# Performance work log

Hardware: AMD Instinct MI355X
Metric: run time of the kernel (lower is better)

The kernel has to match this reference:

```python
import jax, jax.numpy as jnp
import numpy as np
from jax.ops import segment_sum

N = 100000      # nodes
E = 1600000     # edges
G = 128         # graphs in batch
D = 128         # input (embedding) dim
H = 128         # hidden dim
WALK = 16       # random-walk length
PED = 16        # PE embed dim
L = 5           # GNN layers
OUT = 10        # classes
EPS = 1e-5      # batchnorm eps


def setup_inputs() -> dict:
    key = jax.random.key(0)
    ks = jax.random.split(key, 32)
    f = lambda k, shp: (jax.random.normal(k, shp, dtype=jnp.float32) * 0.05)
    inp = {
        'x': jnp.zeros((N,), dtype=jnp.int64) if jax.config.jax_enable_x64 else jnp.zeros((N,), dtype=jnp.int32),
        'edge_index': jax.random.randint(ks[0], (2, E), 0, N),
        'batch': jnp.sort(jax.random.randint(ks[1], (N,), 0, G)),
        'emb_table': f(ks[2], (1, D)),
        'pe_w': f(ks[3], (WALK, PED)), 'pe_b': f(ks[4], (PED,)),
        'proj_w': f(ks[5], (D + PED, H)), 'proj_b': f(ks[6], (H,)),
        'gin_w1': f(ks[7], (L, H, H)), 'gin_b1': f(ks[8], (L, H)),
        'gin_w2': f(ks[9], (L, H, H)), 'gin_b2': f(ks[10], (L, H)),
        'bn_g': jnp.ones((L, H), jnp.float32), 'bn_b': jnp.zeros((L, H), jnp.float32),
        'ffn_w1': f(ks[11], (L, H, 2 * H)), 'ffn_b1': f(ks[12], (L, 2 * H)),
        'ffn_w2': f(ks[13], (L, 2 * H, H)), 'ffn_b2': f(ks[14], (L, H)),
        'ffn_bn_g': jnp.ones((L, H), jnp.float32), 'ffn_bn_b': jnp.zeros((L, H), jnp.float32),
        'out_w1': f(ks[15], (H, H)), 'out_b1': f(ks[16], (H,)),
        'out_w2': f(ks[17], (H, OUT)), 'out_b2': f(ks[18], (OUT,)),
    }
    return inp


def _batchnorm(h, g, b):
    # BatchNorm1d forward with batch statistics (training-mode math)
    mu = jnp.mean(h, axis=0)
    var = jnp.var(h, axis=0)
    return (h - mu) * jax.lax.rsqrt(var + EPS) * g + b


def _forward(emb_table, pe_w, pe_b, proj_w, proj_b, gin_w1, gin_b1, gin_w2, gin_b2,
             bn_g, bn_b, ffn_w1, ffn_b1, ffn_w2, ffn_b2, ffn_bn_g, ffn_bn_b,
             out_w1, out_b1, out_w2, out_b2, x, edge_index, batch):
    h0 = emb_table[x]                                # [N, D] (all indices are 0)

    # ---- RandomWalkPositionalEncoding (vectorized scatter-add per step) ----
    row0, col0 = edge_index[0], edge_index[1]
    loops = jnp.arange(N)
    row = jnp.concatenate([row0, loops])
    col = jnp.concatenate([col0, loops])             # self loops appended
    deg = segment_sum(jnp.ones(row.shape, jnp.float32), col, num_segments=N)
    dinv = jnp.where(deg > 0, jax.lax.rsqrt(jnp.maximum(deg, 1.0)), 0.0)
    norm_e = dinv[row] * dinv[col]                   # [E+N]

    cnt = segment_sum(jnp.ones((N,), jnp.float32), batch, num_segments=G)
    prob = 1.0 / jnp.maximum(cnt, 1.0)[batch]        # per-graph uniform init

    def rw_step(p, _):
        new_p = segment_sum(p[row] * norm_e, col, num_segments=N)
        return new_p * 0.9 + p * 0.1, p

    _, rw = jax.lax.scan(rw_step, prob, None, length=WALK)   # [WALK, N]
    pe = rw.T @ pe_w + pe_b                          # [N, PED]

    # ---- input projection ----
    h = jnp.concatenate([h0, pe], axis=-1) @ proj_w + proj_b # [N, H]

    # ---- stacked GIN layers with BN, residual and FFN (dropout = eval identity) ----
    for i in range(L):
        res = h
        agg = segment_sum(h[row0], col0, num_segments=N) + h  # GIN: (1+eps)x + sum_j x_j, eps=0
        z = jax.nn.relu(agg @ gin_w1[i] + gin_b1[i]) @ gin_w2[i] + gin_b2[i]
        z = jax.nn.relu(_batchnorm(z, bn_g[i], bn_b[i]))
        h = z + res
        res2 = h
        f = jax.nn.relu(h @ ffn_w1[i] + ffn_b1[i]) @ ffn_w2[i] + ffn_b2[i]
        h = _batchnorm(f + res2, ffn_bn_g[i], ffn_bn_b[i])

    # ---- global mean pooling + MLP head ----
    gsum = segment_sum(h, batch, num_segments=G)
    g = gsum / jnp.maximum(cnt, 1.0)[:, None]        # [G, H]
    out = jax.nn.relu(g @ out_w1 + out_b1) @ out_w2 + out_b2
    return out                                        # [G, OUT]


def reference(x, edge_index, batch, emb_table, pe_w, pe_b, proj_w, proj_b,
              gin_w1, gin_b1, gin_w2, gin_b2, bn_g, bn_b, ffn_w1, ffn_b1,
              ffn_w2, ffn_b2, ffn_bn_g, ffn_bn_b, out_w1, out_b1, out_w2, out_b2):
    return _forward(emb_table, pe_w, pe_b, proj_w, proj_b, gin_w1, gin_b1, gin_w2,
                    gin_b2, bn_g, bn_b, ffn_w1, ffn_b1, ffn_w2, ffn_b2,
                    ffn_bn_g, ffn_bn_b, out_w1, out_b1, out_w2, out_b2,
                    x, edge_index, batch)
```

## Files before the change

kernel.cpp:

```cpp
#include <hip/hip_runtime.h>
#include <math.h>

#define NN 100000
#define NE 1600000
#define NG 128
#define HD 128
#define WLK 16
#define NL 5
#define NOUT 10
#define BNEPS 1e-5f
#define CDIV(a,b) (((a)+(b)-1)/(b))

#define NBKT 782
#define NEB 400
#define EPB 4000
#define NSCAN (NBKT*NEB)
#define NSB CDIV(NSCAN,1024)
#define NBM 782

typedef float f32x4 __attribute__((ext_vector_type(4)));
typedef _Float16 f16x8 __attribute__((ext_vector_type(8)));
typedef unsigned short ushort_t;
typedef unsigned int uint_t;

__device__ __forceinline__ ushort_t f2h(float x) {
    union { _Float16 h; ushort_t u; } c;
    c.h = (_Float16)x;
    return c.u;
}
__device__ __forceinline__ float h2f(ushort_t u) {
    union { ushort_t u; _Float16 h; } c;
    c.u = u;
    return (float)c.h;
}

__global__ void k_cnt(const int* __restrict__ batch, int* __restrict__ cnt,
                      int* __restrict__ goff) {
    int g = threadIdx.x;
    if (g >= NG) return;
    int lo0 = 0, hi0 = NN;
    while (lo0 < hi0) { int m = (lo0 + hi0) >> 1; if (batch[m] < g) lo0 = m + 1; else hi0 = m; }
    int lo1 = lo0, hi1 = NN;
    while (lo1 < hi1) { int m = (lo1 + hi1) >> 1; if (batch[m] < g + 1) lo1 = m + 1; else hi1 = m; }
    cnt[g] = lo1 - lo0;
    goff[g] = lo0;
}

__global__ void k_bhist(const int* __restrict__ col0, int* __restrict__ bhist) {
    __shared__ int hist[NBKT];
    for (int i = threadIdx.x; i < NBKT; i += 256) hist[i] = 0;
    __syncthreads();
    int e0 = blockIdx.x * EPB;
    for (int e = e0 + threadIdx.x; e < e0 + EPB; e += 256) atomicAdd(&hist[col0[e] >> 7], 1);
    __syncthreads();
    for (int i = threadIdx.x; i < NBKT; i += 256) bhist[i * NEB + blockIdx.x] = hist[i];
}

__global__ void k_gscan1(const int* __restrict__ in, int* __restrict__ bsum) {
    __shared__ int sm[256];
    int base = blockIdx.x * 1024 + threadIdx.x * 4;
    int s = 0;
#pragma unroll
    for (int i = 0; i < 4; ++i) { int e = base + i; if (e < NSCAN) s += in[e]; }
    sm[threadIdx.x] = s; __syncthreads();
    for (int st = 128; st > 0; st >>= 1) {
        if (threadIdx.x < st) sm[threadIdx.x] += sm[threadIdx.x + st];
        __syncthreads();
    }
    if (threadIdx.x == 0) bsum[blockIdx.x] = sm[0];
}

__global__ void k_scan2(int* __restrict__ blksum, int nblk) {
    __shared__ int sm[512];
    int t = threadIdx.x;
    int x = (t < nblk) ? blksum[t] : 0;
    sm[t] = x; __syncthreads();
    for (int s = 1; s < 512; s <<= 1) {
        int v = (t >= s) ? sm[t - s] : 0;
        __syncthreads();
        sm[t] += v;
        __syncthreads();
    }
    if (t < nblk) blksum[t] = sm[t] - x;
}

__global__ void k_gscan3(const int* __restrict__ in, const int* __restrict__ bsum,
                         int* __restrict__ out) {
    __shared__ int sm[256];
    int t = threadIdx.x;
    int base = blockIdx.x * 1024 + t * 4;
    int v[4]; int s = 0;
#pragma unroll
    for (int i = 0; i < 4; ++i) { int e = base + i; v[i] = (e < NSCAN) ? in[e] : 0; s += v[i]; }
    sm[t] = s; __syncthreads();
    for (int st = 1; st < 256; st <<= 1) {
        int x = (t >= st) ? sm[t - st] : 0;
        __syncthreads();
        sm[t] += x;
        __syncthreads();
    }
    int excl = sm[t] - s + bsum[blockIdx.x];
#pragma unroll
    for (int i = 0; i < 4; ++i) { int e = base + i; if (e < NSCAN) { out[e] = excl; excl += v[i]; } }
}

__global__ void k_escatter(const int* __restrict__ row0, const int* __restrict__ col0,
                           const int* __restrict__ boffs, int2* __restrict__ epair) {
    __shared__ int cur[NBKT];
    for (int i = threadIdx.x; i < NBKT; i += 256) cur[i] = boffs[i * NEB + blockIdx.x];
    __syncthreads();
    int e0 = blockIdx.x * EPB;
    for (int e = e0 + threadIdx.x; e < e0 + EPB; e += 256) {
        int c = col0[e], r = row0[e];
        int pos = atomicAdd(&cur[c >> 7], 1);
        epair[pos] = make_int2(c, r);
    }
}

__global__ void k_bucket(const int2* __restrict__ epair, const int* __restrict__ boffs,
                         int* __restrict__ rowptr, int* __restrict__ deg,
                         int* __restrict__ esrc) {
    __shared__ int cnt_[128], scn[128], cur_[128];
    int bkt = blockIdx.x, t = threadIdx.x;
    int bs = boffs[bkt * NEB];
    int be = (bkt + 1 < NBKT) ? boffs[(bkt + 1) * NEB] : NE;
    if (t < 128) cnt_[t] = 0;
    __syncthreads();
    for (int e = bs + t; e < be; e += 256) atomicAdd(&cnt_[epair[e].x & 127], 1);
    __syncthreads();
    int c = (t < 128) ? cnt_[t] : 0;
    if (t < 128) scn[t] = c;
    __syncthreads();
    for (int st = 1; st < 128; st <<= 1) {
        int x = (t >= st && t < 128) ? scn[t - st] : 0;
        __syncthreads();
        if (t < 128) scn[t] += x;
        __syncthreads();
    }
    if (t < 128) {
        int excl = scn[t] - c;
        int node = bkt * 128 + t;
        if (node < NN) { rowptr[node] = bs + excl; deg[node] = c; }
        cur_[t] = bs + excl;
    }
    if (bkt == NBKT - 1 && t == 0) rowptr[NN] = NE;
    __syncthreads();
    for (int e = bs + t; e < be; e += 256) {
        int2 p = epair[e];
        int pos = atomicAdd(&cur_[p.x & 127], 1);
        esrc[pos] = p.y;
    }
}

__global__ void k_init_pe(const int* __restrict__ deg, const int* __restrict__ batch,
                          const int* __restrict__ cnt, float* __restrict__ dinv,
                          float* __restrict__ p, float* __restrict__ pd) {
    int v = blockIdx.x * 256 + threadIdx.x;
    if (v >= NN) return;
    float dv = rsqrtf((float)(deg[v] + 1));
    dinv[v] = dv;
    float pv = 1.0f / fmaxf((float)cnt[batch[v]], 1.0f);
    p[v] = pv; pd[v] = pv * dv;
}

__global__ void k_rw_step(const float* __restrict__ pin, const float* __restrict__ pdin,
                          const int* __restrict__ rowptr, const int* __restrict__ esrc,
                          const float* __restrict__ dinv, float* __restrict__ rwslice,
                          float* __restrict__ pout, float* __restrict__ pdout) {
    int v = blockIdx.x * 256 + threadIdx.x;
    if (v >= NN) return;
    int b = rowptr[v], e = rowptr[v + 1];
    float a0 = 0.f, a1 = 0.f, a2 = 0.f, a3 = 0.f;
    int i = b;
    for (; i + 4 <= e; i += 4) {
        int s0 = esrc[i], s1 = esrc[i + 1], s2 = esrc[i + 2], s3 = esrc[i + 3];
        a0 += pdin[s0]; a1 += pdin[s1]; a2 += pdin[s2]; a3 += pdin[s3];
    }
    for (; i < e; ++i) a0 += pdin[esrc[i]];
    float s = (a0 + a1) + (a2 + a3);
    float dv = dinv[v];
    float pv = pin[v];
    float np = s * dv + pv * dv * dv;
    float nxt = 0.9f * np + 0.1f * pv;
    rwslice[v] = pv;
    pout[v] = nxt;
    pdout[v] = nxt * dv;
}

__global__ void k_mc1(const float* __restrict__ emb, const float* __restrict__ pe_w,
                      const float* __restrict__ pe_b, const float* __restrict__ proj_w,
                      const float* __restrict__ proj_b, float* __restrict__ M,
                      float* __restrict__ c1, float* __restrict__ bnA0,
                      float* __restrict__ bnB0) {
    int j = threadIdx.x;
    bnA0[j] = 1.f; bnB0[j] = 0.f;
    float c0 = proj_b[j];
    for (int d = 0; d < HD; ++d) c0 += emb[d] * proj_w[d * HD + j];
    for (int w = 0; w < WLK; ++w) c0 += pe_b[w] * proj_w[(HD + w) * HD + j];
    c1[j] = c0;
    for (int s = 0; s < WLK; ++s) {
        float m = 0.f;
        for (int w = 0; w < WLK; ++w) m += pe_w[s * WLK + w] * proj_w[(HD + w) * HD + j];
        M[s * HD + j] = m;
    }
}

__global__ void k_proj(const float* __restrict__ rw, const float* __restrict__ M,
                       const float* __restrict__ c1, uint2* __restrict__ th4) {
    int idx = blockIdx.x * 256 + threadIdx.x;
    if (idx >= NN * 32) return;
    int v = idx >> 5, cg = (idx & 31) * 4;
    float4 acc = *(const float4*)&c1[cg];
#pragma unroll
    for (int s = 0; s < WLK; ++s) {
        float r = rw[s * NN + v];
        float4 m = *(const float4*)&M[s * HD + cg];
        acc.x += r * m.x; acc.y += r * m.y; acc.z += r * m.z; acc.w += r * m.w;
    }
    th4[idx] = make_uint2((uint_t)f2h(acc.x) | ((uint_t)f2h(acc.y) << 16),
                          (uint_t)f2h(acc.z) | ((uint_t)f2h(acc.w) << 16));
}

__global__ void k_prepw(const float* __restrict__ g1, const float* __restrict__ g2,
                        const float* __restrict__ f1, const float* __restrict__ f2,
                        ushort_t* __restrict__ wt1, ushort_t* __restrict__ wt2,
                        ushort_t* __restrict__ wt3, ushort_t* __restrict__ wt4) {
    int i = blockIdx.x * 256 + threadIdx.x;
    if (i < 81920) {
        int l = i >> 14, rem = i & 16383, n = rem >> 7, k = rem & 127;
        wt1[i] = f2h(g1[l * 16384 + k * 128 + n]);
    } else if (i < 163840) {
        int j = i - 81920;
        int l = j >> 14, rem = j & 16383, n = rem >> 7, k = rem & 127;
        wt2[j] = f2h(g2[l * 16384 + k * 128 + n]);
    } else if (i < 327680) {
        int j = i - 163840;
        int l = j >> 15, rem = j & 32767, n = rem >> 7, k = rem & 127;
        wt3[j] = f2h(f1[l * 32768 + k * 256 + n]);
    } else {
        int j = i - 327680;
        int l = j >> 15, rem = j & 32767, n = rem >> 8, k = rem & 255;
        wt4[j] = f2h(f2[l * 32768 + k * 128 + n]);
    }
}

__global__ void k_aggb(const uint_t* __restrict__ th2, const int* __restrict__ rowptr,
                       const int* __restrict__ esrc, const float* __restrict__ bnA0,
                       const float* __restrict__ bnB0, uint_t* __restrict__ aggb2) {
    int wave = threadIdx.x >> 6, lane = threadIdx.x & 63;
    int v = blockIdx.x * 4 + wave;
    if (v >= NN) return;
    uint_t u = th2[(size_t)v * 64 + lane];
    float sx[8], sy[8];
#pragma unroll
    for (int k = 0; k < 8; ++k) { sx[k] = 0.f; sy[k] = 0.f; }
    sx[0] = h2f((ushort_t)(u & 0xFFFFu)); sy[0] = h2f((ushort_t)(u >> 16));
    int b = rowptr[v], e = rowptr[v + 1];
    int i = b;
    for (; i + 8 <= e; i += 8) {
        int idx[8]; uint_t x[8];
#pragma unroll
        for (int k = 0; k < 8; ++k) idx[k] = esrc[i + k];
#pragma unroll
        for (int k = 0; k < 8; ++k) x[k] = th2[(size_t)idx[k] * 64 + lane];
#pragma unroll
        for (int k = 0; k < 8; ++k) {
            sx[k] += h2f((ushort_t)(x[k] & 0xFFFFu));
            sy[k] += h2f((ushort_t)(x[k] >> 16));
        }
    }
    for (; i < e; ++i) {
        uint_t x = th2[(size_t)esrc[i] * 64 + lane];
        sx[0] += h2f((ushort_t)(x & 0xFFFFu)); sy[0] += h2f((ushort_t)(x >> 16));
    }
    float fx = ((sx[0] + sx[1]) + (sx[2] + sx[3])) + ((sx[4] + sx[5]) + (sx[6] + sx[7]));
    float fy = ((sy[0] + sy[1]) + (sy[2] + sy[3])) + ((sy[4] + sy[5]) + (sy[6] + sy[7]));
    float2 A = *(const float2*)&bnA0[lane * 2];
    float2 B = *(const float2*)&bnB0[lane * 2];
    float cf = (float)(e - b + 1);
    float ox = A.x * fx + cf * B.x;
    float oy = A.y * fy + cf * B.y;
    aggb2[(size_t)v * 64 + lane] = (uint_t)f2h(ox) | ((uint_t)f2h(oy) << 16);
}

#define GLDK 136
__global__ __launch_bounds__(256)
void k_gin(const ushort_t* __restrict__ A, const ushort_t* __restrict__ W1T,
           const ushort_t* __restrict__ W2T, const float* __restrict__ b1,
           const float* __restrict__ b2, ushort_t* __restrict__ z2h,
           float* __restrict__ partS, float* __restrict__ partQ) {
    __shared__ ushort_t As[128 * GLDK];
    __shared__ ushort_t Ws[64 * GLDK];
    __shared__ float sS[128], sQ[128];
    const int tid = threadIdx.x;
    const int w = tid >> 6, l = tid & 63;
    const int lm = l & 15, lq = l >> 4;
    const int rw0 = w * 32;
    const int vr0 = blockIdx.x * 128;
    if (tid < 128) { sS[tid] = 0.f; sQ[tid] = 0.f; }

#pragma unroll
    for (int it = 0; it < 8; ++it) {
        int f = it * 256 + tid;
        int row = f >> 4, sl = f & 15;
        uint4 a = make_uint4(0, 0, 0, 0);
        int vr = vr0 + row;
        if (vr < NN) a = *(const uint4*)&A[(size_t)vr * HD + sl * 8];
        *(uint4*)&As[row * GLDK + sl * 8] = a;
    }

    f32x4 z1a[2][2][4] = {};
    for (int c = 0; c < 2; ++c) {
        __syncthreads();
#pragma unroll
        for (int it = 0; it < 4; ++it) {
            int f = it * 256 + tid;
            int row = f >> 4, sl = f & 15;
            *(uint4*)&Ws[row * GLDK + sl * 8] =
                *(const uint4*)&W1T[(size_t)(c * 64 + row) * HD + sl * 8];
        }
        __syncthreads();
#pragma unroll
        for (int kk = 0; kk < 128; kk += 32) {
            f16x8 af[2], bf[4];
#pragma unroll
            for (int i = 0; i < 2; ++i)
                af[i] = *(const f16x8*)&As[(rw0 + i * 16 + lm) * GLDK + kk + lq * 8];
#pragma unroll
            for (int j = 0; j < 4; ++j)
                bf[j] = *(const f16x8*)&Ws[(j * 16 + lm) * GLDK + kk + lq * 8];
#pragma unroll
            for (int i = 0; i < 2; ++i)
#pragma unroll
                for (int j = 0; j < 4; ++j)
                    z1a[c][i][j] = __builtin_amdgcn_mfma_f32_16x16x32_f16(af[i], bf[j], z1a[c][i][j], 0, 0, 0);
        }
    }
    __syncthreads();

#pragma unroll
    for (int c = 0; c < 2; ++c)
#pragma unroll
        for (int j = 0; j < 4; ++j) {
            int col = c * 64 + j * 16 + lm;
            float bj = b1[col];
#pragma unroll
            for (int i = 0; i < 2; ++i)
#pragma unroll
                for (int r = 0; r < 4; ++r) {
                    int row = rw0 + i * 16 + lq * 4 + r;
                    As[row * GLDK + col] = f2h(fmaxf(z1a[c][i][j][r] + bj, 0.f));
                }
        }

    f32x4 z2a[2][2][4] = {};
    for (int c2 = 0; c2 < 2; ++c2) {
        __syncthreads();
#pragma unroll
        for (int it = 0; it < 4; ++it) {
            int f = it * 256 + tid;
            int row = f >> 4, sl = f & 15;
            *(uint4*)&Ws[row * GLDK + sl * 8] =
                *(const uint4*)&W2T[(size_t)(c2 * 64 + row) * HD + sl * 8];
        }
        __syncthreads();
#pragma unroll
        for (int kk = 0; kk < 128; kk += 32) {
            f16x8 af[2], bf[4];
#pragma unroll
            for (int i = 0; i < 2; ++i)
                af[i] = *(const f16x8*)&As[(rw0 + i * 16 + lm) * GLDK + kk + lq * 8];
#pragma unroll
            for (int j = 0; j < 4; ++j)
                bf[j] = *(const f16x8*)&Ws[(j * 16 + lm) * GLDK + kk + lq * 8];
#pragma unroll
            for (int i = 0; i < 2; ++i)
#pragma unroll
                for (int j = 0; j < 4; ++j)
                    z2a[c2][i][j] = __builtin_amdgcn_mfma_f32_16x16x32_f16(af[i], bf[j], z2a[c2][i][j], 0, 0, 0);
        }
    }

    float ls[2][4] = {}, lsq[2][4] = {};
#pragma unroll
    for (int c2 = 0; c2 < 2; ++c2)
#pragma unroll
        for (int j = 0; j < 4; ++j) {
            int col = c2 * 64 + j * 16 + lm;
            float bj = b2[col];
#pragma unroll
            for (int i = 0; i < 2; ++i)
#pragma unroll
                for (int r = 0; r < 4; ++r) {
                    int vr = vr0 + rw0 + i * 16 + lq * 4 + r;
                    if (vr < NN) {
                        float x = z2a[c2][i][j][r] + bj;
                        ls[c2][j] += x; lsq[c2][j] += x * x;
                        z2h[(size_t)vr * HD + col] = f2h(x);
                    }
                }
        }
#pragma unroll
    for (int c2 = 0; c2 < 2; ++c2)
#pragma unroll
        for (int j = 0; j < 4; ++j) {
            atomicAdd(&sS[c2 * 64 + j * 16 + lm], ls[c2][j]);
            atomicAdd(&sQ[c2 * 64 + j * 16 + lm], lsq[c2][j]);
        }
    __syncthreads();
    if (tid < 128) {
        partS[(size_t)tid * NBM + blockIdx.x] = sS[tid];
        partQ[(size_t)tid * NBM + blockIdx.x] = sQ[tid];
    }
}

__global__ __launch_bounds__(256)
void k_ffn1(const ushort_t* __restrict__ th, const ushort_t* __restrict__ z2h,
            const ushort_t* __restrict__ W3T, const float* __restrict__ b3,
            const float* __restrict__ bnA0, const float* __restrict__ bnB0,
            const float* __restrict__ bnA1, const float* __restrict__ bnB1,
            float* __restrict__ hmid, ushort_t* __restrict__ f1h) {
    __shared__ ushort_t As[128 * GLDK];
    __shared__ ushort_t Ws[64 * GLDK];
    __shared__ float sA0[128], sB0[128], sA1[128], sB1[128];
    const int tid = threadIdx.x;
    const int w = tid >> 6, l = tid & 63;
    const int lm = l & 15, lq = l >> 4;
    const int rw0 = w * 32;
    const int vr0 = blockIdx.x * 128;

    if (tid < 128) {
        sA0[tid] = bnA0[tid]; sB0[tid] = bnB0[tid];
        sA1[tid] = bnA1[tid]; sB1[tid] = bnB1[tid];
    }
    __syncthreads();

#pragma unroll
    for (int it = 0; it < 8; ++it) {
        int f = it * 256 + tid;
        int row = f >> 4, sl = f & 15;
        int vr = vr0 + row;
        uint4 o = make_uint4(0, 0, 0, 0);
        if (vr < NN) {
            uint4 tv = *(const uint4*)&th[(size_t)vr * HD + sl * 8];
            uint4 zv = *(const uint4*)&z2h[(size_t)vr * HD + sl * 8];
            uint_t tu[4] = {tv.x, tv.y, tv.z, tv.w};
            uint_t zu[4] = {zv.x, zv.y, zv.z, zv.w};
            float hm[8];
            uint_t ou[4];
#pragma unroll
            for (int m = 0; m < 4; ++m) {
                int ch0 = sl * 8 + m * 2;
                float t0 = h2f((ushort_t)(tu[m] & 0xFFFFu));
                float t1 = h2f((ushort_t)(tu[m] >> 16));
                float z0 = h2f((ushort_t)(zu[m] & 0xFFFFu));
                float z1 = h2f((ushort_t)(zu[m] >> 16));
                float h0 = sA0[ch0] * t0 + sB0[ch0] + fmaxf(sA1[ch0] * z0 + sB1[ch0], 0.f);
                float h1 = sA0[ch0 + 1] * t1 + sB0[ch0 + 1] + fmaxf(sA1[ch0 + 1] * z1 + sB1[ch0 + 1], 0.f);
                hm[m * 2] = h0; hm[m * 2 + 1] = h1;
                ou[m] = (uint_t)f2h(h0) | ((uint_t)f2h(h1) << 16);
            }
            o = make_uint4(ou[0], ou[1], ou[2], ou[3]);
            *(float4*)&hmid[(size_t)vr * HD + sl * 8] = make_float4(hm[0], hm[1], hm[2], hm[3]);
            *(float4*)&hmid[(size_t)vr * HD + sl * 8 + 4] = make_float4(hm[4], hm[5], hm[6], hm[7]);
        }
        *(uint4*)&As[row * GLDK + sl * 8] = o;
    }

    for (int c = 0; c < 4; ++c) {
        __syncthreads();
#pragma unroll
        for (int it = 0; it < 4; ++it) {
            int f = it * 256 + tid;
            int row = f >> 4, sl = f & 15;
            *(uint4*)&Ws[row * GLDK + sl * 8] =
                *(const uint4*)&W3T[(size_t)(c * 64 + row) * HD + sl * 8];
        }
        __syncthreads();
        f32x4 acc[2][4] = {};
#pragma unroll
        for (int kk = 0; kk < 128; kk += 32) {
            f16x8 af[2], bf[4];
#pragma unroll
            for (int i = 0; i < 2; ++i)
                af[i] = *(const f16x8*)&As[(rw0 + i * 16 + lm) * GLDK + kk + lq * 8];
#pragma unroll
            for (int j = 0; j < 4; ++j)
                bf[j] = *(const f16x8*)&Ws[(j * 16 + lm) * GLDK + kk + lq * 8];
#pragma unroll
            for (int i = 0; i < 2; ++i)
#pragma unroll
                for (int j = 0; j < 4; ++j)
                    acc[i][j] = __builtin_amdgcn_mfma_f32_16x16x32_f16(af[i], bf[j], acc[i][j], 0, 0, 0);
        }
#pragma unroll
        for (int j = 0; j < 4; ++j) {
            int col = c * 64 + j * 16 + lm;
            float bj = b3[col];
#pragma unroll
            for (int i = 0; i < 2; ++i)
#pragma unroll
                for (int r = 0; r < 4; ++r) {
                    int vr = vr0 + rw0 + i * 16 + lq * 4 + r;
                    if (vr < NN)
                        f1h[(size_t)vr * 256 + col] = f2h(fmaxf(acc[i][j][r] + bj, 0.f));
                }
        }
    }
}

template <int K, bool RELU, bool OUTH16, bool ADDRES, bool DOSTATS>
__global__ __launch_bounds__(256, 2)
void k_mgemm(const ushort_t* __restrict__ A, const ushort_t* __restrict__ WT,
             const float* __restrict__ bias, ushort_t* __restrict__ Ch,
             float* __restrict__ Cf, const float* __restrict__ res,
             float* __restrict__ partS, float* __restrict__ partQ, int ncols) {
    constexpr int LDK = 72;
    __shared__ ushort_t As[128 * LDK];
    __shared__ ushort_t Ws[128 * LDK];
    __shared__ float sS[128], sQ[128];
    const int tid = threadIdx.x;
    const int w = tid >> 6, l = tid & 63;
    const int lm = l & 15, lq = l >> 4;
    const int rb = (w >> 1) * 64, cbw = (w & 1) * 64;
    const int vr0 = blockIdx.x * 128;
    const int cb = blockIdx.y * 128;
    f32x4 acc[4][4] = {};

    for (int kt = 0; kt < K / 64; ++kt) {
        __syncthreads();
#pragma unroll
        for (int it = 0; it < 4; ++it) {
            int f = it * 256 + tid;
            int row = f >> 3, sl = f & 7;
            uint4 a = make_uint4(0, 0, 0, 0);
            int vr = vr0 + row;
            if (vr < NN) a = *(const uint4*)&A[(size_t)vr * K + kt * 64 + sl * 8];
            *(uint4*)&As[row * LDK + sl * 8] = a;
            uint4 wv = *(const uint4*)&WT[(size_t)(cb + row) * K + kt * 64 + sl * 8];
            *(uint4*)&Ws[row * LDK + sl * 8] = wv;
        }
        __syncthreads();
#pragma unroll
        for (int kk = 0; kk < 64; kk += 32) {
            f16x8 af[4], bf[4];
#pragma unroll
            for (int i = 0; i < 4; ++i)
                af[i] = *(const f16x8*)&As[(rb + i * 16 + lm) * LDK + kk + lq * 8];
#pragma unroll
            for (int j = 0; j < 4; ++j)
                bf[j] = *(const f16x8*)&Ws[(cbw + j * 16 + lm) * LDK + kk + lq * 8];
#pragma unroll
            for (int i = 0; i < 4; ++i)
#pragma unroll
                for (int j = 0; j < 4; ++j)
                    acc[i][j] = __builtin_amdgcn_mfma_f32_16x16x32_f16(af[i], bf[j], acc[i][j], 0, 0, 0);
        }
    }

    float bcol[4];
#pragma unroll
    for (int j = 0; j < 4; ++j) bcol[j] = bias[cb + cbw + j * 16 + lm];
    if (DOSTATS && tid < 128) { sS[tid] = 0.f; sQ[tid] = 0.f; }
    __syncthreads();
    float ls[4] = {0, 0, 0, 0}, lsq[4] = {0, 0, 0, 0};
#pragma unroll
    for (int i = 0; i < 4; ++i) {
#pragma unroll
        for (int r = 0; r < 4; ++r) {
            int vr = vr0 + rb + i * 16 + lq * 4 + r;
            if (vr < NN) {
#pragma unroll
                for (int j = 0; j < 4; ++j) {
                    float x = acc[i][j][r] + bcol[j];
                    if (RELU) x = fmaxf(x, 0.f);
                    int c = cb + cbw + j * 16 + lm;
                    if (ADDRES) x += res[(size_t)vr * ncols + c];
                    if (DOSTATS) { ls[j] += x; lsq[j] += x * x; }
                    if (OUTH16) Ch[(size_t)vr * ncols + c] = f2h(x);
                    else        Cf[(size_t)vr * ncols + c] = x;
                }
            }
        }
    }
    if (DOSTATS) {
#pragma unroll
        for (int j = 0; j < 4; ++j) {
            atomicAdd(&sS[cbw + j * 16 + lm], ls[j]);
            atomicAdd(&sQ[cbw + j * 16 + lm], lsq[j]);
        }
        __syncthreads();
        if (tid < 128) {
            partS[(size_t)(cb + tid) * NBM + blockIdx.x] = sS[tid];
            partQ[(size_t)(cb + tid) * NBM + blockIdx.x] = sQ[tid];
        }
    }
}

__global__ void k_bnparm(const float* __restrict__ partS, const float* __restrict__ partQ,
                         const float* __restrict__ g, const float* __restrict__ b,
                         float* __restrict__ bnA, float* __restrict__ bnB) {
    __shared__ float smS[256], smQ[256];
    int c = blockIdx.x, t = threadIdx.x;
    float s = 0.f, q = 0.f;
    for (int i = t; i < NBM; i += 256) {
        s += partS[(size_t)c * NBM + i];
        q += partQ[(size_t)c * NBM + i];
    }
    smS[t] = s; smQ[t] = q; __syncthreads();
    for (int st = 128; st > 0; st >>= 1) {
        if (t < st) { smS[t] += smS[t + st]; smQ[t] += smQ[t + st]; }
        __syncthreads();
    }
    if (t == 0) {
        float mu = smS[0] * (1.0f / NN);
        float var = smQ[0] * (1.0f / NN) - mu * mu;
        float inv = rsqrtf(var + BNEPS);
        float a = g[c] * inv;
        bnA[c] = a;
        bnB[c] = b[c] - mu * a;
    }
}

__global__ void k_pool(const uint2* __restrict__ th4, const int* __restrict__ goff,
                       const int* __restrict__ cnt, float* __restrict__ gsum) {
    __shared__ float4 sm[256];
    int g = blockIdx.x >> 2, sub = blockIdx.x & 3;
    int n0 = goff[g], n = cnt[g];
    int cg = threadIdx.x & 31, rl = threadIdx.x >> 5;
    float4 acc = make_float4(0.f, 0.f, 0.f, 0.f);
    for (int r = sub * 8 + rl; r < n; r += 32) {
        uint2 v = th4[(size_t)(n0 + r) * 32 + cg];
        acc.x += h2f((ushort_t)(v.x & 0xFFFFu));
        acc.y += h2f((ushort_t)(v.x >> 16));
        acc.z += h2f((ushort_t)(v.y & 0xFFFFu));
        acc.w += h2f((ushort_t)(v.y >> 16));
    }
    sm[threadIdx.x] = acc; __syncthreads();
    for (int st = 128; st >= 32; st >>= 1) {
        if (threadIdx.x < st) {
            float4 o = sm[threadIdx.x + st];
            sm[threadIdx.x].x += o.x; sm[threadIdx.x].y += o.y;
            sm[threadIdx.x].z += o.z; sm[threadIdx.x].w += o.w;
        }
        __syncthreads();
    }
    if (threadIdx.x < 32) {
        float4 v = sm[threadIdx.x];
        atomicAdd(&gsum[g * HD + cg * 4 + 0], v.x);
        atomicAdd(&gsum[g * HD + cg * 4 + 1], v.y);
        atomicAdd(&gsum[g * HD + cg * 4 + 2], v.z);
        atomicAdd(&gsum[g * HD + cg * 4 + 3], v.w);
    }
}

__global__ void k_head(const float* __restrict__ gsum, const int* __restrict__ cnt,
                       const float* __restrict__ bnA0, const float* __restrict__ bnB0,
                       const float* __restrict__ w1, const float* __restrict__ b1,
                       const float* __restrict__ w2, const float* __restrict__ b2,
                       float* __restrict__ out) {
    __shared__ float gv[HD], av[HD];
    int gid = blockIdx.x, t = threadIdx.x;
    float c = fmaxf((float)cnt[gid], 1.0f);
    gv[t] = bnA0[t] * (gsum[gid * HD + t] / c) + bnB0[t];
    __syncthreads();
    float a = b1[t];
    for (int k = 0; k < HD; ++k) a += gv[k] * w1[k * HD + t];
    av[t] = fmaxf(a, 0.f);
    __syncthreads();
    if (t < NOUT) {
        float o = b2[t];
        for (int k = 0; k < HD; ++k) o += av[k] * w2[k * NOUT + t];
        out[gid * NOUT + t] = o;
    }
}

static constexpr size_t AL(size_t x) { return (x + 511) & ~(size_t)511; }
static constexpr size_t OFF_HMID   = 0;
static constexpr size_t OFF_TH     = OFF_HMID   + AL((size_t)NN * HD * 4);
static constexpr size_t OFF_SHARE  = OFF_TH     + AL((size_t)NN * HD * 2);
static constexpr size_t SZ_SHARE   = AL((size_t)NN * 256 * 2);
static constexpr size_t OFF_Z2     = OFF_SHARE  + SZ_SHARE;
static constexpr size_t OFF_RW     = OFF_Z2     + AL((size_t)NN * HD * 2);
static constexpr size_t OFF_P0     = OFF_RW     + AL((size_t)WLK * NN * 4);
static constexpr size_t OFF_P1     = OFF_P0     + AL((size_t)NN * 4);
static constexpr size_t OFF_PD0    = OFF_P1     + AL((size_t)NN * 4);
static constexpr size_t OFF_PD1    = OFF_PD0    + AL((size_t)NN * 4);
static constexpr size_t OFF_DINV   = OFF_PD1    + AL((size_t)NN * 4);
static constexpr size_t OFF_ESRC   = OFF_DINV   + AL((size_t)NN * 4);
static constexpr size_t OFF_ROWPTR = OFF_ESRC   + AL((size_t)NE * 4);
static constexpr size_t OFF_DEG    = OFF_ROWPTR + AL((size_t)(NN + 1) * 4);
static constexpr size_t OFF_BHIST  = OFF_DEG    + AL((size_t)NN * 4);
static constexpr size_t OFF_BOFFS  = OFF_BHIST  + AL((size_t)NSCAN * 4);
static constexpr size_t OFF_BSUM   = OFF_BOFFS  + AL((size_t)NSCAN * 4);
static constexpr size_t OFF_WT1    = OFF_BSUM   + AL(512 * 4);
static constexpr size_t OFF_WT2    = OFF_WT1    + AL((size_t)5 * 16384 * 2);
static constexpr size_t OFF_WT3    = OFF_WT2    + AL((size_t)5 * 16384 * 2);
static constexpr size_t OFF_WT4    = OFF_WT3    + AL((size_t)5 * 32768 * 2);
static constexpr size_t OFF_PARTS  = OFF_WT4    + AL((size_t)5 * 32768 * 2);
static constexpr size_t OFF_PARTQ  = OFF_PARTS  + AL((size_t)128 * NBM * 4);
static constexpr size_t OFF_BNA0   = OFF_PARTQ  + AL((size_t)128 * NBM * 4);
static constexpr size_t OFF_BNB0   = OFF_BNA0   + AL(128 * 4);
static constexpr size_t OFF_BNA1   = OFF_BNB0   + AL(128 * 4);
static constexpr size_t OFF_BNB1   = OFF_BNA1   + AL(128 * 4);
static constexpr size_t OFF_M      = OFF_BNB1   + AL(128 * 4);
static constexpr size_t OFF_C1     = OFF_M      + AL((size_t)WLK * HD * 4);
static constexpr size_t OFF_CNT    = OFF_C1     + AL(HD * 4);
static constexpr size_t OFF_GOFF   = OFF_CNT    + AL(NG * 4);
static constexpr size_t OFF_GSUM   = OFF_GOFF   + AL(NG * 4);
static constexpr size_t ZERO_BYTES = (size_t)NG * HD * 4;

extern "C" void kernel_launch(void* const* d_in, const int* in_sizes, int n_in,
                              void* d_out, int out_size, void* d_ws, size_t ws_size,
                              hipStream_t stream) {
    const int* eidx = (const int*)d_in[1];
    const int* row0 = eidx;
    const int* col0 = eidx + NE;
    const int* batch = (const int*)d_in[2];
    const float* emb = (const float*)d_in[3];
    const float* pe_w = (const float*)d_in[4];
    const float* pe_b = (const float*)d_in[5];
    const float* proj_w = (const float*)d_in[6];
    const float* proj_b = (const float*)d_in[7];
    const float* gin_w1 = (const float*)d_in[8];
    const float* gin_b1 = (const float*)d_in[9];
    const float* gin_w2 = (const float*)d_in[10];
    const float* gin_b2 = (const float*)d_in[11];
    const float* bn_g = (const float*)d_in[12];
    const float* bn_b = (const float*)d_in[13];
    const float* ffn_w1 = (const float*)d_in[14];
    const float* ffn_b1 = (const float*)d_in[15];
    const float* ffn_w2 = (const float*)d_in[16];
    const float* ffn_b2 = (const float*)d_in[17];
    const float* ffn_bn_g = (const float*)d_in[18];
    const float* ffn_bn_b = (const float*)d_in[19];
    const float* out_w1 = (const float*)d_in[20];
    const float* out_b1 = (const float*)d_in[21];
    const float* out_w2 = (const float*)d_in[22];
    const float* out_b2 = (const float*)d_in[23];
    float* out = (float*)d_out;

    char* ws = (char*)d_ws;
    float*    hmid  = (float*)(ws + OFF_HMID);
    ushort_t* th    = (ushort_t*)(ws + OFF_TH);
    ushort_t* aggh  = (ushort_t*)(ws + OFF_SHARE);
    ushort_t* f1h   = (ushort_t*)(ws + OFF_SHARE);
    ushort_t* z2h   = (ushort_t*)(ws + OFF_Z2);
    int2*     epair = (int2*)(ws + OFF_SHARE);
    float*    rw    = (float*)(ws + OFF_RW);
    float*    p0    = (float*)(ws + OFF_P0);
    float*    p1    = (float*)(ws + OFF_P1);
    float*    pd0   = (float*)(ws + OFF_PD0);
    float*    pd1   = (float*)(ws + OFF_PD1);
    float*    dinv  = (float*)(ws + OFF_DINV);
    int*      esrc  = (int*)(ws + OFF_ESRC);
    int*      rowptr= (int*)(ws + OFF_ROWPTR);
    int*      deg   = (int*)(ws + OFF_DEG);
    int*      bhist = (int*)(ws + OFF_BHIST);
    int*      boffs = (int*)(ws + OFF_BOFFS);
    int*      bsum  = (int*)(ws + OFF_BSUM);
    ushort_t* wt1   = (ushort_t*)(ws + OFF_WT1);
    ushort_t* wt2   = (ushort_t*)(ws + OFF_WT2);
    ushort_t* wt3   = (ushort_t*)(ws + OFF_WT3);
    ushort_t* wt4   = (ushort_t*)(ws + OFF_WT4);
    float*    partS = (float*)(ws + OFF_PARTS);
    float*    partQ = (float*)(ws + OFF_PARTQ);
    float*    bnA0  = (float*)(ws + OFF_BNA0);
    float*    bnB0  = (float*)(ws + OFF_BNB0);
    float*    bnA1  = (float*)(ws + OFF_BNA1);
    float*    bnB1  = (float*)(ws + OFF_BNB1);
    float*    M     = (float*)(ws + OFF_M);
    float*    c1    = (float*)(ws + OFF_C1);
    int*      cnt   = (int*)(ws + OFF_CNT);
    int*      goff  = (int*)(ws + OFF_GOFF);
    float*    gsum  = (float*)(ws + OFF_GSUM);

    const int NB = CDIV(NN, 256);
    const int NBV = CDIV(NN * 32, 256);

    hipMemsetAsync(ws + OFF_GSUM, 0, ZERO_BYTES, stream);

    k_cnt<<<1, 128, 0, stream>>>(batch, cnt, goff);
    k_bhist<<<NEB, 256, 0, stream>>>(col0, bhist);
    k_gscan1<<<NSB, 256, 0, stream>>>(bhist, bsum);
    k_scan2<<<1, 512, 0, stream>>>(bsum, NSB);
    k_gscan3<<<NSB, 256, 0, stream>>>(bhist, bsum, boffs);
    k_escatter<<<NEB, 256, 0, stream>>>(row0, col0, boffs, epair);
    k_bucket<<<NBKT, 256, 0, stream>>>(epair, boffs, rowptr, deg, esrc);

    k_init_pe<<<NB, 256, 0, stream>>>(deg, batch, cnt, dinv, p0, pd0);
    k_mc1<<<1, 128, 0, stream>>>(emb, pe_w, pe_b, proj_w, proj_b, M, c1, bnA0, bnB0);
    k_prepw<<<1920, 256, 0, stream>>>(gin_w1, gin_w2, ffn_w1, ffn_w2, wt1, wt2, wt3, wt4);
    for (int s = 0; s < WLK; ++s) {
        const float* pin = (s & 1) ? p1 : p0;
        const float* pdin = (s & 1) ? pd1 : pd0;
        float* pout = (s & 1) ? p0 : p1;
        float* pdout = (s & 1) ? pd0 : pd1;
        k_rw_step<<<NB, 256, 0, stream>>>(pin, pdin, rowptr, esrc, dinv,
                                          rw + (size_t)s * NN, pout, pdout);
    }
    k_proj<<<NBV, 256, 0, stream>>>(rw, M, c1, (uint2*)th);

    dim3 g1(NBM, 1);
    for (int i = 0; i < NL; ++i) {
        k_aggb<<<CDIV(NN, 4), 256, 0, stream>>>((const uint_t*)th, rowptr, esrc,
                                                bnA0, bnB0, (uint_t*)aggh);
        k_gin<<<NBM, 256, 0, stream>>>(aggh, wt1 + (size_t)i * 16384, wt2 + (size_t)i * 16384,
                                       gin_b1 + i * HD, gin_b2 + i * HD, z2h, partS, partQ);
        k_bnparm<<<128, 256, 0, stream>>>(partS, partQ, bn_g + i * HD, bn_b + i * HD, bnA1, bnB1);
        k_ffn1<<<NBM, 256, 0, stream>>>(th, z2h, wt3 + (size_t)i * 32768, ffn_b1 + i * 256,
                                        bnA0, bnB0, bnA1, bnB1, hmid, f1h);
        k_mgemm<256, false, true, true, true><<<g1, 256, 0, stream>>>(
            f1h, wt4 + (size_t)i * 32768, ffn_b2 + i * HD, th, nullptr, hmid,
            partS, partQ, 128);
        k_bnparm<<<128, 256, 0, stream>>>(partS, partQ, ffn_bn_g + i * HD, ffn_bn_b + i * HD,
                                          bnA0, bnB0);
    }

    k_pool<<<NG * 4, 256, 0, stream>>>((const uint2*)th, goff, cnt, gsum);
    k_head<<<NG, 128, 0, stream>>>(gsum, cnt, bnA0, bnB0, out_w1, out_b1, out_w2, out_b2, out);
}
```

Before: 1.585 ms.

## Fuse neighbor aggregation into GIN GEMM and recompute FFN residual instead of storing fp32

```diff
diff --git a/kernel.cpp b/kernel.cpp
--- a/kernel.cpp
+++ b/kernel.cpp
@@ -170,14 +170,19 @@
     int v = blockIdx.x * 256 + threadIdx.x;
     if (v >= NN) return;
     int b = rowptr[v], e = rowptr[v + 1];
-    float a0 = 0.f, a1 = 0.f, a2 = 0.f, a3 = 0.f;
+    float a[8];
+#pragma unroll
+    for (int k = 0; k < 8; ++k) a[k] = 0.f;
     int i = b;
-    for (; i + 4 <= e; i += 4) {
-        int s0 = esrc[i], s1 = esrc[i + 1], s2 = esrc[i + 2], s3 = esrc[i + 3];
-        a0 += pdin[s0]; a1 += pdin[s1]; a2 += pdin[s2]; a3 += pdin[s3];
-    }
-    for (; i < e; ++i) a0 += pdin[esrc[i]];
-    float s = (a0 + a1) + (a2 + a3);
+    for (; i + 8 <= e; i += 8) {
+        int s[8];
+#pragma unroll
+        for (int k = 0; k < 8; ++k) s[k] = esrc[i + k];
+#pragma unroll
+        for (int k = 0; k < 8; ++k) a[k] += pdin[s[k]];
+    }
+    for (; i < e; ++i) a[0] += pdin[esrc[i]];
+    float s = ((a[0] + a[1]) + (a[2] + a[3])) + ((a[4] + a[5]) + (a[6] + a[7]));
     float dv = dinv[v];
     float pv = pin[v];
     float np = s * dv + pv * dv * dv;
@@ -244,51 +249,15 @@
     }
 }
 
-__global__ void k_aggb(const uint_t* __restrict__ th2, const int* __restrict__ rowptr,
-                       const int* __restrict__ esrc, const float* __restrict__ bnA0,
-                       const float* __restrict__ bnB0, uint_t* __restrict__ aggb2) {
-    int wave = threadIdx.x >> 6, lane = threadIdx.x & 63;
-    int v = blockIdx.x * 4 + wave;
-    if (v >= NN) return;
-    uint_t u = th2[(size_t)v * 64 + lane];
-    float sx[8], sy[8];
-#pragma unroll
-    for (int k = 0; k < 8; ++k) { sx[k] = 0.f; sy[k] = 0.f; }
-    sx[0] = h2f((ushort_t)(u & 0xFFFFu)); sy[0] = h2f((ushort_t)(u >> 16));
-    int b = rowptr[v], e = rowptr[v + 1];
-    int i = b;
-    for (; i + 8 <= e; i += 8) {
-        int idx[8]; uint_t x[8];
-#pragma unroll
-        for (int k = 0; k < 8; ++k) idx[k] = esrc[i + k];
-#pragma unroll
-        for (int k = 0; k < 8; ++k) x[k] = th2[(size_t)idx[k] * 64 + lane];
-#pragma unroll
-        for (int k = 0; k < 8; ++k) {
-            sx[k] += h2f((ushort_t)(x[k] & 0xFFFFu));
-            sy[k] += h2f((ushort_t)(x[k] >> 16));
-        }
-    }
-    for (; i < e; ++i) {
-        uint_t x = th2[(size_t)esrc[i] * 64 + lane];
-        sx[0] += h2f((ushort_t)(x & 0xFFFFu)); sy[0] += h2f((ushort_t)(x >> 16));
-    }
-    float fx = ((sx[0] + sx[1]) + (sx[2] + sx[3])) + ((sx[4] + sx[5]) + (sx[6] + sx[7]));
-    float fy = ((sy[0] + sy[1]) + (sy[2] + sy[3])) + ((sy[4] + sy[5]) + (sy[6] + sy[7]));
-    float2 A = *(const float2*)&bnA0[lane * 2];
-    float2 B = *(const float2*)&bnB0[lane * 2];
-    float cf = (float)(e - b + 1);
-    float ox = A.x * fx + cf * B.x;
-    float oy = A.y * fy + cf * B.y;
-    aggb2[(size_t)v * 64 + lane] = (uint_t)f2h(ox) | ((uint_t)f2h(oy) << 16);
-}
-
 #define GLDK 136
 __global__ __launch_bounds__(256)
-void k_gin(const ushort_t* __restrict__ A, const ushort_t* __restrict__ W1T,
-           const ushort_t* __restrict__ W2T, const float* __restrict__ b1,
-           const float* __restrict__ b2, ushort_t* __restrict__ z2h,
-           float* __restrict__ partS, float* __restrict__ partQ) {
+void k_gin(const uint_t* __restrict__ th2, const int* __restrict__ rowptr,
+           const int* __restrict__ esrc, const float* __restrict__ bnA0,
+           const float* __restrict__ bnB0,
+           const ushort_t* __restrict__ W1T, const ushort_t* __restrict__ W2T,
+           const float* __restrict__ b1, const float* __restrict__ b2,
+           ushort_t* __restrict__ z2h, float* __restrict__ partS,
+           float* __restrict__ partQ) {
     __shared__ ushort_t As[128 * GLDK];
     __shared__ ushort_t Ws[64 * GLDK];
     __shared__ float sS[128], sQ[128];
@@ -299,14 +268,42 @@
     const int vr0 = blockIdx.x * 128;
     if (tid < 128) { sS[tid] = 0.f; sQ[tid] = 0.f; }
 
-#pragma unroll
-    for (int it = 0; it < 8; ++it) {
-        int f = it * 256 + tid;
-        int row = f >> 4, sl = f & 15;
-        uint4 a = make_uint4(0, 0, 0, 0);
-        int vr = vr0 + row;
-        if (vr < NN) a = *(const uint4*)&A[(size_t)vr * HD + sl * 8];
-        *(uint4*)&As[row * GLDK + sl * 8] = a;
+    const float2 Afc = *(const float2*)&bnA0[l * 2];
+    const float2 Bfc = *(const float2*)&bnB0[l * 2];
+    for (int rr = 0; rr < 32; ++rr) {
+        int v = vr0 + rw0 + rr;
+        uint_t outw = 0;
+        if (v < NN) {
+            uint_t u = th2[(size_t)v * 64 + l];
+            float sx[8], sy[8];
+#pragma unroll
+            for (int k = 0; k < 8; ++k) { sx[k] = 0.f; sy[k] = 0.f; }
+            sx[0] = h2f((ushort_t)(u & 0xFFFFu)); sy[0] = h2f((ushort_t)(u >> 16));
+            int b = rowptr[v], e = rowptr[v + 1];
+            int i = b;
+            for (; i + 8 <= e; i += 8) {
+                int idx[8]; uint_t x[8];
+#pragma unroll
+                for (int k = 0; k < 8; ++k) idx[k] = esrc[i + k];
+#pragma unroll
+                for (int k = 0; k < 8; ++k) x[k] = th2[(size_t)idx[k] * 64 + l];
+#pragma unroll
+                for (int k = 0; k < 8; ++k) {
+                    sx[k] += h2f((ushort_t)(x[k] & 0xFFFFu));
+                    sy[k] += h2f((ushort_t)(x[k] >> 16));
+                }
+            }
+            for (; i < e; ++i) {
+                uint_t x = th2[(size_t)esrc[i] * 64 + l];
+                sx[0] += h2f((ushort_t)(x & 0xFFFFu)); sy[0] += h2f((ushort_t)(x >> 16));
+            }
+            float fx = ((sx[0] + sx[1]) + (sx[2] + sx[3])) + ((sx[4] + sx[5]) + (sx[6] + sx[7]));
+            float fy = ((sy[0] + sy[1]) + (sy[2] + sy[3])) + ((sy[4] + sy[5]) + (sy[6] + sy[7]));
+            float cf = (float)(e - b + 1);
+            outw = (uint_t)f2h(Afc.x * fx + cf * Bfc.x) |
+                   ((uint_t)f2h(Afc.y * fy + cf * Bfc.y) << 16);
+        }
+        *(uint_t*)&As[(rw0 + rr) * GLDK + l * 2] = outw;
     }
 
     f32x4 z1a[2][2][4] = {};
@@ -419,7 +416,7 @@
             const ushort_t* __restrict__ W3T, const float* __restrict__ b3,
             const float* __restrict__ bnA0, const float* __restrict__ bnB0,
             const float* __restrict__ bnA1, const float* __restrict__ bnB1,
-            float* __restrict__ hmid, ushort_t* __restrict__ f1h) {
+            ushort_t* __restrict__ f1h) {
     __shared__ ushort_t As[128 * GLDK];
     __shared__ ushort_t Ws[64 * GLDK];
     __shared__ float sA0[128], sB0[128], sA1[128], sB1[128];
@@ -446,7 +443,6 @@
             uint4 zv = *(const uint4*)&z2h[(size_t)vr * HD + sl * 8];
             uint_t tu[4] = {tv.x, tv.y, tv.z, tv.w};
             uint_t zu[4] = {zv.x, zv.y, zv.z, zv.w};
-            float hm[8];
             uint_t ou[4];
 #pragma unroll
             for (int m = 0; m < 4; ++m) {
@@ -457,12 +453,9 @@
                 float z1 = h2f((ushort_t)(zu[m] >> 16));
                 float h0 = sA0[ch0] * t0 + sB0[ch0] + fmaxf(sA1[ch0] * z0 + sB1[ch0], 0.f);
                 float h1 = sA0[ch0 + 1] * t1 + sB0[ch0 + 1] + fmaxf(sA1[ch0 + 1] * z1 + sB1[ch0 + 1], 0.f);
-                hm[m * 2] = h0; hm[m * 2 + 1] = h1;
                 ou[m] = (uint_t)f2h(h0) | ((uint_t)f2h(h1) << 16);
             }
             o = make_uint4(ou[0], ou[1], ou[2], ou[3]);
-            *(float4*)&hmid[(size_t)vr * HD + sl * 8] = make_float4(hm[0], hm[1], hm[2], hm[3]);
-            *(float4*)&hmid[(size_t)vr * HD + sl * 8 + 4] = make_float4(hm[4], hm[5], hm[6], hm[7]);
         }
         *(uint4*)&As[row * GLDK + sl * 8] = o;
     }
@@ -509,12 +502,13 @@
     }
 }
 
-template <int K, bool RELU, bool OUTH16, bool ADDRES, bool DOSTATS>
 __global__ __launch_bounds__(256, 2)
-void k_mgemm(const ushort_t* __restrict__ A, const ushort_t* __restrict__ WT,
-             const float* __restrict__ bias, ushort_t* __restrict__ Ch,
-             float* __restrict__ Cf, const float* __restrict__ res,
-             float* __restrict__ partS, float* __restrict__ partQ, int ncols) {
+void k_ffn2(const ushort_t* __restrict__ f1h, const ushort_t* __restrict__ WT,
+            const float* __restrict__ bias, ushort_t* __restrict__ th,
+            const ushort_t* __restrict__ z2h,
+            const float* __restrict__ bnA0, const float* __restrict__ bnB0,
+            const float* __restrict__ bnA1, const float* __restrict__ bnB1,
+            float* __restrict__ partS, float* __restrict__ partQ) {
     constexpr int LDK = 72;
     __shared__ ushort_t As[128 * LDK];
     __shared__ ushort_t Ws[128 * LDK];
@@ -524,10 +518,9 @@
     const int lm = l & 15, lq = l >> 4;
     const int rb = (w >> 1) * 64, cbw = (w & 1) * 64;
     const int vr0 = blockIdx.x * 128;
-    const int cb = blockIdx.y * 128;
     f32x4 acc[4][4] = {};
 
-    for (int kt = 0; kt < K / 64; ++kt) {
+    for (int kt = 0; kt < 4; ++kt) {
         __syncthreads();
 #pragma unroll
         for (int it = 0; it < 4; ++it) {
@@ -535,9 +528,9 @@
             int row = f >> 3, sl = f & 7;
             uint4 a = make_uint4(0, 0, 0, 0);
             int vr = vr0 + row;
-            if (vr < NN) a = *(const uint4*)&A[(size_t)vr * K + kt * 64 + sl * 8];
+            if (vr < NN) a = *(const uint4*)&f1h[(size_t)vr * 256 + kt * 64 + sl * 8];
             *(uint4*)&As[row * LDK + sl * 8] = a;
-            uint4 wv = *(const uint4*)&WT[(size_t)(cb + row) * K + kt * 64 + sl * 8];
+            uint4 wv = *(const uint4*)&WT[(size_t)row * 256 + kt * 64 + sl * 8];
             *(uint4*)&Ws[row * LDK + sl * 8] = wv;
         }
         __syncthreads();
@@ -558,10 +551,15 @@
         }
     }
 
-    float bcol[4];
-#pragma unroll
-    for (int j = 0; j < 4; ++j) bcol[j] = bias[cb + cbw + j * 16 + lm];
-    if (DOSTATS && tid < 128) { sS[tid] = 0.f; sQ[tid] = 0.f; }
+    float bcol[4], a0c[4], b0c[4], a1c[4], b1c[4];
+#pragma unroll
+    for (int j = 0; j < 4; ++j) {
+        int c = cbw + j * 16 + lm;
+        bcol[j] = bias[c];
+        a0c[j] = bnA0[c]; b0c[j] = bnB0[c];
+        a1c[j] = bnA1[c]; b1c[j] = bnB1[c];
+    }
+    if (tid < 128) { sS[tid] = 0.f; sQ[tid] = 0.f; }
     __syncthreads();
     float ls[4] = {0, 0, 0, 0}, lsq[4] = {0, 0, 0, 0};
 #pragma unroll
@@ -572,28 +570,26 @@
             if (vr < NN) {
 #pragma unroll
                 for (int j = 0; j < 4; ++j) {
-                    float x = acc[i][j][r] + bcol[j];
-                    if (RELU) x = fmaxf(x, 0.f);
-                    int c = cb + cbw + j * 16 + lm;
-                    if (ADDRES) x += res[(size_t)vr * ncols + c];
-                    if (DOSTATS) { ls[j] += x; lsq[j] += x * x; }
-                    if (OUTH16) Ch[(size_t)vr * ncols + c] = f2h(x);
-                    else        Cf[(size_t)vr * ncols + c] = x;
+                    int c = cbw + j * 16 + lm;
+                    float t = h2f(th[(size_t)vr * HD + c]);
+                    float z = h2f(z2h[(size_t)vr * HD + c]);
+                    float resv = a0c[j] * t + b0c[j] + fmaxf(a1c[j] * z + b1c[j], 0.f);
+                    float x = acc[i][j][r] + bcol[j] + resv;
+                    ls[j] += x; lsq[j] += x * x;
+                    th[(size_t)vr * HD + c] = f2h(x);
                 }
             }
         }
     }
-    if (DOSTATS) {
-#pragma unroll
-        for (int j = 0; j < 4; ++j) {
-            atomicAdd(&sS[cbw + j * 16 + lm], ls[j]);
-            atomicAdd(&sQ[cbw + j * 16 + lm], lsq[j]);
-        }
-        __syncthreads();
-        if (tid < 128) {
-            partS[(size_t)(cb + tid) * NBM + blockIdx.x] = sS[tid];
-            partQ[(size_t)(cb + tid) * NBM + blockIdx.x] = sQ[tid];
-        }
+#pragma unroll
+    for (int j = 0; j < 4; ++j) {
+        atomicAdd(&sS[cbw + j * 16 + lm], ls[j]);
+        atomicAdd(&sQ[cbw + j * 16 + lm], lsq[j]);
+    }
+    __syncthreads();
+    if (tid < 128) {
+        partS[(size_t)tid * NBM + blockIdx.x] = sS[tid];
+        partQ[(size_t)tid * NBM + blockIdx.x] = sQ[tid];
     }
 }
 
@@ -676,8 +672,7 @@
 }
 
 static constexpr size_t AL(size_t x) { return (x + 511) & ~(size_t)511; }
-static constexpr size_t OFF_HMID   = 0;
-static constexpr size_t OFF_TH     = OFF_HMID   + AL((size_t)NN * HD * 4);
+static constexpr size_t OFF_TH     = 0;
 static constexpr size_t OFF_SHARE  = OFF_TH     + AL((size_t)NN * HD * 2);
 static constexpr size_t SZ_SHARE   = AL((size_t)NN * 256 * 2);
 static constexpr size_t OFF_Z2     = OFF_SHARE  + SZ_SHARE;
@@ -741,12 +736,10 @@
     float* out = (float*)d_out;
 
     char* ws = (char*)d_ws;
-    float*    hmid  = (float*)(ws + OFF_HMID);
     ushort_t* th    = (ushort_t*)(ws + OFF_TH);
-    ushort_t* aggh  = (ushort_t*)(ws + OFF_SHARE);
     ushort_t* f1h   = (ushort_t*)(ws + OFF_SHARE);
+    int2*     epair = (int2*)(ws + OFF_SHARE);
     ushort_t* z2h   = (ushort_t*)(ws + OFF_Z2);
-    int2*     epair = (int2*)(ws + OFF_SHARE);
     float*    rw    = (float*)(ws + OFF_RW);
     float*    p0    = (float*)(ws + OFF_P0);
     float*    p1    = (float*)(ws + OFF_P1);
@@ -801,18 +794,15 @@
     }
     k_proj<<<NBV, 256, 0, stream>>>(rw, M, c1, (uint2*)th);
 
-    dim3 g1(NBM, 1);
     for (int i = 0; i < NL; ++i) {
-        k_aggb<<<CDIV(NN, 4), 256, 0, stream>>>((const uint_t*)th, rowptr, esrc,
-                                                bnA0, bnB0, (uint_t*)aggh);
-        k_gin<<<NBM, 256, 0, stream>>>(aggh, wt1 + (size_t)i * 16384, wt2 + (size_t)i * 16384,
+        k_gin<<<NBM, 256, 0, stream>>>((const uint_t*)th, rowptr, esrc, bnA0, bnB0,
+                                       wt1 + (size_t)i * 16384, wt2 + (size_t)i * 16384,
                                        gin_b1 + i * HD, gin_b2 + i * HD, z2h, partS, partQ);
         k_bnparm<<<128, 256, 0, stream>>>(partS, partQ, bn_g + i * HD, bn_b + i * HD, bnA1, bnB1);
         k_ffn1<<<NBM, 256, 0, stream>>>(th, z2h, wt3 + (size_t)i * 32768, ffn_b1 + i * 256,
-                                        bnA0, bnB0, bnA1, bnB1, hmid, f1h);
-        k_mgemm<256, false, true, true, true><<<g1, 256, 0, stream>>>(
-            f1h, wt4 + (size_t)i * 32768, ffn_b2 + i * HD, th, nullptr, hmid,
-            partS, partQ, 128);
+                                        bnA0, bnB0, bnA1, bnB1, f1h);
+        k_ffn2<<<NBM, 256, 0, stream>>>(f1h, wt4 + (size_t)i * 32768, ffn_b2 + i * HD,
+                                        th, z2h, bnA0, bnB0, bnA1, bnB1, partS, partQ);
         k_bnparm<<<128, 256, 0, stream>>>(partS, partQ, ffn_bn_g + i * HD, ffn_bn_b + i * HD,
                                           bnA0, bnB0);
     }
```

Measured after the change: 2.208 ms. 39.3% more time.
